# Kernel optimization log

Measured on AMD Instinct MI355X. Metric: run time of the kernel, lower is better.

## Reference

```python
import jax, jax.numpy as jnp
import numpy as np

N_NODES = 50000
N_EDGES = 800000
IN_CH, HID, OUT_CH, HEADS = 128, 32, 32, 8
NEG_SLOPE = 0.2


def setup_inputs() -> dict:
    key = jax.random.key(0)
    ks = jax.random.split(key, 20)
    x = jax.random.normal(ks[0], (N_NODES, IN_CH), dtype=jnp.float32)
    edge_index = jax.random.randint(ks[1], (2, N_EDGES), 0, N_NODES, dtype=jnp.int64)
    s = 0.1
    # encoder layer 1: in -> hid, heads=8 (concat)
    W1 = jax.random.normal(ks[2], (IN_CH, HEADS * HID), jnp.float32) * s
    as1 = jax.random.normal(ks[3], (HEADS, HID), jnp.float32) * s
    ad1 = jax.random.normal(ks[4], (HEADS, HID), jnp.float32) * s
    b1 = jnp.zeros((HEADS * HID,), jnp.float32)
    # encoder layer 2: hid*heads -> out, heads=1
    W2 = jax.random.normal(ks[5], (HEADS * HID, OUT_CH), jnp.float32) * s
    as2 = jax.random.normal(ks[6], (1, OUT_CH), jnp.float32) * s
    ad2 = jax.random.normal(ks[7], (1, OUT_CH), jnp.float32) * s
    b2 = jnp.zeros((OUT_CH,), jnp.float32)
    # decoder layer 1: out -> hid, heads=8 (concat)
    W3 = jax.random.normal(ks[8], (OUT_CH, HEADS * HID), jnp.float32) * s
    as3 = jax.random.normal(ks[9], (HEADS, HID), jnp.float32) * s
    ad3 = jax.random.normal(ks[10], (HEADS, HID), jnp.float32) * s
    b3 = jnp.zeros((HEADS * HID,), jnp.float32)
    # decoder layer 2: hid*heads -> in, heads=1
    W4 = jax.random.normal(ks[11], (HEADS * HID, IN_CH), jnp.float32) * s
    as4 = jax.random.normal(ks[12], (1, IN_CH), jnp.float32) * s
    ad4 = jax.random.normal(ks[13], (1, IN_CH), jnp.float32) * s
    b4 = jnp.zeros((IN_CH,), jnp.float32)
    return dict(x=x, edge_index=edge_index, W1=W1, as1=as1, ad1=ad1, b1=b1,
                W2=W2, as2=as2, ad2=ad2, b2=b2, W3=W3, as3=as3, ad3=ad3, b3=b3,
                W4=W4, as4=as4, ad4=ad4, b4=b4)


def gat_conv(x, src, dst, W, a_src, a_dst, b, heads, ch):
    # PyG GATConv: h = xW, e_ij = LeakyReLU(a_src.h_j + a_dst.h_i), softmax over incoming edges of i
    h = (x @ W).reshape(-1, heads, ch)                       # [N, H, C]
    al_s = jnp.sum(h * a_src[None], axis=-1)                 # [N, H]
    al_d = jnp.sum(h * a_dst[None], axis=-1)                 # [N, H]
    e = jax.nn.leaky_relu(al_s[src] + al_d[dst], NEG_SLOPE)  # [E, H]
    emax = jax.ops.segment_max(e, dst, num_segments=N_NODES)
    ee = jnp.exp(e - emax[dst])
    denom = jax.ops.segment_sum(ee, dst, num_segments=N_NODES)
    alpha = ee / denom[dst]                                  # [E, H]
    msg = alpha[:, :, None] * h[src]                         # [E, H, C]
    out = jax.ops.segment_sum(msg, dst, num_segments=N_NODES)  # [N, H, C]
    return out.reshape(N_NODES, heads * ch) + b


def reference(x, edge_index, W1, as1, ad1, b1, W2, as2, ad2, b2,
              W3, as3, ad3, b3, W4, as4, ad4, b4):
    # add self loops (PyG default add_self_loops=True)
    loop = jnp.arange(N_NODES, dtype=edge_index.dtype)
    src = jnp.concatenate([edge_index[0], loop])
    dst = jnp.concatenate([edge_index[1], loop])
    # encode
    z = gat_conv(x, src, dst, W1, as1, ad1, b1, HEADS, HID)
    z = jax.nn.relu(z)
    z = gat_conv(z, src, dst, W2, as2, ad2, b2, 1, OUT_CH)
    # decode
    r = gat_conv(z, src, dst, W3, as3, ad3, b3, HEADS, HID)
    r = jax.nn.relu(r)
    r = gat_conv(r, src, dst, W4, as4, ad4, b4, 1, IN_CH)
    return r
```

## Files before the change

kernel.cpp:

```cpp
#include <hip/hip_runtime.h>
#include <math.h>

#define N_NODES 50000
#define N_EDGES 800000
#define N_TOT   850000
#define NSB     ((N_NODES + 255) / 256)

typedef __attribute__((ext_vector_type(8))) short short8;
typedef __attribute__((ext_vector_type(4))) float floatx4;

__device__ __forceinline__ unsigned int pack_bf16x2(float a, float b) {
    unsigned ua = __float_as_uint(a);
    unsigned ub = __float_as_uint(b);
    ua += 0x7fff + ((ua >> 16) & 1);
    ub += 0x7fff + ((ub >> 16) & 1);
    return (ua >> 16) | (ub & 0xffff0000u);
}
__device__ __forceinline__ unsigned short pack_bf16(float a) {
    unsigned ua = __float_as_uint(a);
    ua += 0x7fff + ((ua >> 16) & 1);
    return (unsigned short)(ua >> 16);
}
__device__ __forceinline__ float bf16_lo(unsigned u) { return __uint_as_float(u << 16); }
__device__ __forceinline__ float bf16_hi(unsigned u) { return __uint_as_float(u & 0xffff0000u); }

__global__ void zero_int_kernel(int* p, int n) {
    int i = blockIdx.x * blockDim.x + threadIdx.x;
    if (i < n) p[i] = 0;
}

__global__ void deg_hist_kernel(const int* __restrict__ ei, int* __restrict__ deg) {
    int e = blockIdx.x * blockDim.x + threadIdx.x;
    if (e >= N_TOT) return;
    int dst = (e < N_EDGES) ? ei[N_EDGES + e] : (e - N_EDGES);
    atomicAdd(&deg[dst], 1);
}

__global__ void block_scan_kernel(const int* __restrict__ deg, int* __restrict__ part,
                                  int* __restrict__ bsum) {
    __shared__ int tmp[256];
    int t = threadIdx.x;
    int i = blockIdx.x * 256 + t;
    int v = (i < N_NODES) ? deg[i] : 0;
    tmp[t] = v;
    __syncthreads();
    for (int d = 1; d < 256; d <<= 1) {
        int u = (t >= d) ? tmp[t - d] : 0;
        __syncthreads();
        tmp[t] += u;
        __syncthreads();
    }
    if (i < N_NODES) part[i] = tmp[t] - v;
    if (t == 255) bsum[blockIdx.x] = tmp[255];
}

__global__ void scan_bsum_kernel(int* __restrict__ bsum) {
    __shared__ int tmp[256];
    int t = threadIdx.x;
    int v = (t < NSB) ? bsum[t] : 0;
    tmp[t] = v;
    __syncthreads();
    for (int d = 1; d < 256; d <<= 1) {
        int u = (t >= d) ? tmp[t - d] : 0;
        __syncthreads();
        tmp[t] += u;
        __syncthreads();
    }
    if (t < NSB) bsum[t] = tmp[t] - v;
}

__global__ void finalize_off_kernel(const int* __restrict__ part, const int* __restrict__ bsum,
                                    int* __restrict__ off, int* __restrict__ cursor) {
    int i = blockIdx.x * 256 + threadIdx.x;
    if (i < N_NODES) {
        int o = part[i] + bsum[blockIdx.x];
        off[i] = o;
        cursor[i] = o;
    }
    if (i == 0) off[N_NODES] = N_TOT;
}

__global__ void fill_csr_kernel(const int* __restrict__ ei, int* __restrict__ cursor,
                                int* __restrict__ csr_src) {
    int e = blockIdx.x * blockDim.x + threadIdx.x;
    if (e >= N_TOT) return;
    int src, dst;
    if (e < N_EDGES) { src = ei[e]; dst = ei[N_EDGES + e]; }
    else             { src = dst = e - N_EDGES; }
    int pos = atomicAdd(&cursor[dst], 1);
    csr_src[pos] = src;
}

__global__ void wconv_kernel(const float* __restrict__ W1, const float* __restrict__ W2,
                             const float* __restrict__ W3, const float* __restrict__ W4,
                             unsigned short* __restrict__ T1, unsigned short* __restrict__ T2,
                             unsigned short* __restrict__ T3, unsigned short* __restrict__ T4) {
    int i = blockIdx.x * 256 + threadIdx.x;
    const float* W; unsigned short* T; int K, N, idx;
    if      (i < 32768) { W = W1; T = T1; K = 128; N = 256; idx = i; }
    else if (i < 40960) { W = W2; T = T2; K = 256; N = 32;  idx = i - 32768; }
    else if (i < 49152) { W = W3; T = T3; K = 32;  N = 256; idx = i - 40960; }
    else if (i < 81920) { W = W4; T = T4; K = 256; N = 128; idx = i - 49152; }
    else return;
    int n = idx / K, k = idx % K;
    T[idx] = pack_bf16(W[(size_t)k * N + n]);
}

template<int Cin, int Cout, int H, int C, int NPB, int NW_N, bool IN_BF16>
__global__ void gemm_mfma_kernel(const void* __restrict__ xin,
                                 const unsigned short* __restrict__ Wt,
                                 const float* __restrict__ a_src, const float* __restrict__ a_dst,
                                 unsigned short* __restrict__ hb,
                                 float* __restrict__ al_s, float* __restrict__ al_d) {
    constexpr int NW_M = 4 / NW_N;
    constexpr int MT_W = (NPB / 16) / NW_M;
    constexpr int NT_W = (Cout / 16) / NW_N;
    constexpr int AS   = Cin + 8;
    constexpr int SP   = Cout + 4;
    __shared__ unsigned short xs[NPB * AS];
    __shared__ float hs[NPB * SP];
    int tid = threadIdx.x;
    int n0  = blockIdx.x * NPB;

    if (IN_BF16) {
        for (int i = tid; i < NPB * Cin / 8; i += 256) {
            int n = i / (Cin / 8), k8 = i % (Cin / 8);
            uint4 q = make_uint4(0u, 0u, 0u, 0u);
            if (n0 + n < N_NODES)
                q = ((const uint4*)((const unsigned short*)xin + (size_t)(n0 + n) * Cin))[k8];
            *(uint4*)(xs + n * AS + k8 * 8) = q;
        }
    } else {
        for (int i = tid; i < NPB * Cin / 4; i += 256) {
            int n = i / (Cin / 4), k4 = i % (Cin / 4);
            float4 v = make_float4(0.f, 0.f, 0.f, 0.f);
            if (n0 + n < N_NODES)
                v = ((const float4*)((const float*)xin + (size_t)(n0 + n) * Cin))[k4];
            uint2 p;
            p.x = pack_bf16x2(v.x, v.y);
            p.y = pack_bf16x2(v.z, v.w);
            *(uint2*)(xs + n * AS + k4 * 4) = p;
        }
    }
    __syncthreads();

    int w = tid >> 6, lane = tid & 63;
    int q = lane >> 4, l16 = lane & 15;
    int wm = w / NW_N, wn = w % NW_N;
    int mbase = wm * MT_W * 16;
    int nbase = wn * NT_W * 16;

    floatx4 acc[MT_W][NT_W];
#pragma unroll
    for (int mt = 0; mt < MT_W; mt++)
#pragma unroll
        for (int nt = 0; nt < NT_W; nt++) acc[mt][nt] = (floatx4){0.f, 0.f, 0.f, 0.f};

#pragma unroll
    for (int k0 = 0; k0 < Cin; k0 += 32) {
        short8 a[MT_W], b[NT_W];
#pragma unroll
        for (int mt = 0; mt < MT_W; mt++)
            a[mt] = *(const short8*)(xs + (mbase + mt * 16 + l16) * AS + k0 + q * 8);
#pragma unroll
        for (int nt = 0; nt < NT_W; nt++)
            b[nt] = *(const short8*)(Wt + (size_t)(nbase + nt * 16 + l16) * Cin + k0 + q * 8);
#pragma unroll
        for (int mt = 0; mt < MT_W; mt++)
#pragma unroll
            for (int nt = 0; nt < NT_W; nt++)
                acc[mt][nt] = __builtin_amdgcn_mfma_f32_16x16x32_bf16(a[mt], b[nt], acc[mt][nt], 0, 0, 0);
    }

#pragma unroll
    for (int mt = 0; mt < MT_W; mt++)
#pragma unroll
        for (int nt = 0; nt < NT_W; nt++)
#pragma unroll
            for (int r = 0; r < 4; r++) {
                int nl = mbase + mt * 16 + q * 4 + r;
                int ch = nbase + nt * 16 + l16;
                hs[nl * SP + ch] = acc[mt][nt][r];
            }
    __syncthreads();

    constexpr int TPN = Cout / 32;
    constexpr int TPH = (C > 32) ? (C / 32) : 1;
    if (tid < NPB * TPN) {
        int node = tid / TPN, sub = tid % TPN;
        int gn = n0 + node;
        int head = (sub * 32) / C;
        int coff = (sub * 32) % C;
        const float* hrow = hs + node * SP + sub * 32;
        const float* ap = a_src + head * C + coff;
        const float* dp = a_dst + head * C + coff;
        float ps = 0.f, pd = 0.f;
#pragma unroll
        for (int c4 = 0; c4 < 8; c4++) {
            float4 hv = *(const float4*)(hrow + c4 * 4);
            float4 av = *(const float4*)(ap + c4 * 4);
            float4 dv = *(const float4*)(dp + c4 * 4);
            ps += hv.x * av.x + hv.y * av.y + hv.z * av.z + hv.w * av.w;
            pd += hv.x * dv.x + hv.y * dv.y + hv.z * dv.z + hv.w * dv.w;
        }
        uint4 o0, o1;
        {
            float4 h0 = *(const float4*)(hrow + 0);
            float4 h1 = *(const float4*)(hrow + 4);
            float4 h2 = *(const float4*)(hrow + 8);
            float4 h3 = *(const float4*)(hrow + 12);
            o0.x = pack_bf16x2(h0.x, h0.y); o0.y = pack_bf16x2(h0.z, h0.w);
            o0.z = pack_bf16x2(h1.x, h1.y); o0.w = pack_bf16x2(h1.z, h1.w);
            o1.x = pack_bf16x2(h2.x, h2.y); o1.y = pack_bf16x2(h2.z, h2.w);
            o1.z = pack_bf16x2(h3.x, h3.y); o1.w = pack_bf16x2(h3.z, h3.w);
        }
        uint4 o2, o3;
        {
            float4 h0 = *(const float4*)(hrow + 16);
            float4 h1 = *(const float4*)(hrow + 20);
            float4 h2 = *(const float4*)(hrow + 24);
            float4 h3 = *(const float4*)(hrow + 28);
            o2.x = pack_bf16x2(h0.x, h0.y); o2.y = pack_bf16x2(h0.z, h0.w);
            o2.z = pack_bf16x2(h1.x, h1.y); o2.w = pack_bf16x2(h1.z, h1.w);
            o3.x = pack_bf16x2(h2.x, h2.y); o3.y = pack_bf16x2(h2.z, h2.w);
            o3.z = pack_bf16x2(h3.x, h3.y); o3.w = pack_bf16x2(h3.z, h3.w);
        }
        if (gn < N_NODES) {
            uint2* dst = (uint2*)(hb + (size_t)gn * Cout + sub * 32);
            dst[0] = make_uint2(o0.x, o0.y); dst[1] = make_uint2(o0.z, o0.w);
            dst[2] = make_uint2(o1.x, o1.y); dst[3] = make_uint2(o1.z, o1.w);
            dst[4] = make_uint2(o2.x, o2.y); dst[5] = make_uint2(o2.z, o2.w);
            dst[6] = make_uint2(o3.x, o3.y); dst[7] = make_uint2(o3.z, o3.w);
        }
        if (TPH > 1) {
#pragma unroll
            for (int k = 1; k < TPH; k <<= 1) {
                ps += __shfl_xor(ps, k, 64);
                pd += __shfl_xor(pd, k, 64);
            }
            if ((sub % TPH) == 0 && gn < N_NODES) {
                al_s[gn * H + head] = ps;
                al_d[gn * H + head] = pd;
            }
        } else {
            if (gn < N_NODES) {
                al_s[gn * H + head] = ps;
                al_d[gn * H + head] = pd;
            }
        }
    }
}

template<int H, int C, bool RELU, bool OUT_BF16>
__launch_bounds__(256, 6)
__global__ void gat_agg_kernel(const unsigned short* __restrict__ hb,
                               const float* __restrict__ al_s,
                               const float* __restrict__ al_d, const int* __restrict__ off,
                               const int* __restrict__ csr_src, const float* __restrict__ bias,
                               void* __restrict__ out) {
    constexpr int HC  = H * C;
    constexpr int G   = HC / 4;
    constexpr int SUB = G / H;
    constexpr int EB  = (SUB > 8) ? 8 : SUB;
    constexpr int NPW = 64 / G;
    constexpr int NPB = 4 * NPW;

    int tid  = threadIdx.x;
    int wid  = tid >> 6;
    int lane = tid & 63;
    int gi   = lane / G;
    int g    = lane % G;
    int node = blockIdx.x * NPB + wid * NPW + gi;
    if (node >= N_NODES) return;

    int head = g / SUB;
    int es   = g % EB;
    int nb   = lane & ~(G - 1);
    int r0 = off[node], r1 = off[node + 1];
    float ald = al_d[node * H + head];

    const uint2* hb2 = (const uint2*)hb;
    float4 acc = make_float4(0.f, 0.f, 0.f, 0.f);
    float wsum = 0.f;

    int j0 = r0;
    int idx0 = j0 + es;
    int sC = csr_src[(idx0 < r1) ? idx0 : (r1 - 1)];
    float eC = al_s[sC * H + head] + ald;

    for (; j0 + EB <= r1; j0 += EB) {
        int idxn = j0 + EB + es;
        int sN = csr_src[(idxn < r1) ? idxn : (r1 - 1)];
        float eL = fmaxf(eC, 0.2f * eC);
        float wC = __expf(eL);
        float eN = al_s[sN * H + head] + ald;
#pragma unroll
        for (int u = 0; u < EB; u++) {
            float wu = __shfl(wC, nb + head * EB + u, 64);
            int su = (NPW == 1) ? __builtin_amdgcn_readlane(sC, u)
                                : __shfl(sC, nb + u, 64);
            uint2 q = hb2[(size_t)su * G + g];
            wsum += wu;
            acc.x += wu * bf16_lo(q.x); acc.y += wu * bf16_hi(q.x);
            acc.z += wu * bf16_lo(q.y); acc.w += wu * bf16_hi(q.y);
        }
        sC = sN; eC = eN;
    }
    if (j0 < r1) {
        bool valid = (j0 + es) < r1;
        float eL = fmaxf(eC, 0.2f * eC);
        float wC = valid ? __expf(eL) : 0.f;
#pragma unroll
        for (int u = 0; u < EB; u++) {
            float wu = __shfl(wC, nb + head * EB + u, 64);
            if (wu != 0.f) {
                int su = (NPW == 1) ? __builtin_amdgcn_readlane(sC, u)
                                    : __shfl(sC, nb + u, 64);
                uint2 q = hb2[(size_t)su * G + g];
                wsum += wu;
                acc.x += wu * bf16_lo(q.x); acc.y += wu * bf16_hi(q.x);
                acc.z += wu * bf16_lo(q.y); acc.w += wu * bf16_hi(q.y);
            }
        }
    }

    float inv = 1.f / wsum;
    float4 bv = ((const float4*)bias)[g];
    acc.x = acc.x * inv + bv.x;
    acc.y = acc.y * inv + bv.y;
    acc.z = acc.z * inv + bv.z;
    acc.w = acc.w * inv + bv.w;
    if (RELU) {
        acc.x = fmaxf(acc.x, 0.f); acc.y = fmaxf(acc.y, 0.f);
        acc.z = fmaxf(acc.z, 0.f); acc.w = fmaxf(acc.w, 0.f);
    }
    if (OUT_BF16) {
        uint2 p;
        p.x = pack_bf16x2(acc.x, acc.y);
        p.y = pack_bf16x2(acc.z, acc.w);
        ((uint2*)out)[(size_t)node * (HC / 4) + g] = p;
    } else {
        ((float4*)out)[(size_t)node * (HC / 4) + g] = acc;
    }
}

extern "C" void kernel_launch(void* const* d_in, const int* in_sizes, int n_in,
                              void* d_out, int out_size, void* d_ws, size_t ws_size,
                              hipStream_t stream) {
    const float* x   = (const float*)d_in[0];
    const int*   ei  = (const int*)d_in[1];
    const float* W1  = (const float*)d_in[2];
    const float* as1 = (const float*)d_in[3];
    const float* ad1 = (const float*)d_in[4];
    const float* b1  = (const float*)d_in[5];
    const float* W2  = (const float*)d_in[6];
    const float* as2 = (const float*)d_in[7];
    const float* ad2 = (const float*)d_in[8];
    const float* b2  = (const float*)d_in[9];
    const float* W3  = (const float*)d_in[10];
    const float* as3 = (const float*)d_in[11];
    const float* ad3 = (const float*)d_in[12];
    const float* b3  = (const float*)d_in[13];
    const float* W4  = (const float*)d_in[14];
    const float* as4 = (const float*)d_in[15];
    const float* ad4 = (const float*)d_in[16];
    const float* b4  = (const float*)d_in[17];

    char* ws = (char*)d_ws;
    size_t o = 0;
    auto alloc = [&](size_t bytes) -> void* {
        void* p = ws + o;
        o = (o + bytes + 255) & ~(size_t)255;
        return p;
    };
    unsigned short* feat_a  = (unsigned short*)alloc((size_t)N_NODES * 256 * 2);
    unsigned short* feat_b  = (unsigned short*)alloc((size_t)N_NODES * 32 * 2);
    unsigned short* h_buf   = (unsigned short*)alloc((size_t)N_NODES * 256 * 2);
    float*          al_s    = (float*)alloc((size_t)N_NODES * 8 * 4);
    float*          al_d    = (float*)alloc((size_t)N_NODES * 8 * 4);
    int*            deg     = (int*)alloc((size_t)(N_NODES + 1) * 4);
    int*            off     = (int*)alloc((size_t)(N_NODES + 1) * 4);
    int*            cursor  = (int*)alloc((size_t)N_NODES * 4);
    int*            part    = (int*)alloc((size_t)N_NODES * 4);
    int*            bsum    = (int*)alloc((size_t)256 * 4);
    int*            csr_src = (int*)alloc((size_t)N_TOT * 4);
    unsigned short* w1t     = (unsigned short*)alloc(32768 * 2);
    unsigned short* w2t     = (unsigned short*)alloc(8192 * 2);
    unsigned short* w3t     = (unsigned short*)alloc(8192 * 2);
    unsigned short* w4t     = (unsigned short*)alloc(32768 * 2);

    const int TPB = 256;
    int nb_nodes = (N_NODES + TPB - 1) / TPB;
    int nb_edges = (N_TOT + TPB - 1) / TPB;

    zero_int_kernel<<<nb_nodes, TPB, 0, stream>>>(deg, N_NODES);
    wconv_kernel<<<320, TPB, 0, stream>>>(W1, W2, W3, W4, w1t, w2t, w3t, w4t);
    deg_hist_kernel<<<nb_edges, TPB, 0, stream>>>(ei, deg);
    block_scan_kernel<<<NSB, TPB, 0, stream>>>(deg, part, bsum);
    scan_bsum_kernel<<<1, TPB, 0, stream>>>(bsum);
    finalize_off_kernel<<<NSB, TPB, 0, stream>>>(part, bsum, off, cursor);
    fill_csr_kernel<<<nb_edges, TPB, 0, stream>>>(ei, cursor, csr_src);

    auto agg_blocks = [](int hc) { return (N_NODES * (hc / 4) + 255) / 256; };

    gemm_mfma_kernel<128, 256, 8, 32, 32, 4, false>
        <<<(N_NODES + 31) / 32, TPB, 0, stream>>>(x, w1t, as1, ad1, h_buf, al_s, al_d);
    gat_agg_kernel<8, 32, true, true><<<agg_blocks(256), TPB, 0, stream>>>(h_buf, al_s, al_d, off, csr_src, b1, feat_a);

    gemm_mfma_kernel<256, 32, 1, 32, 64, 2, true>
        <<<(N_NODES + 63) / 64, TPB, 0, stream>>>(feat_a, w2t, as2, ad2, h_buf, al_s, al_d);
    gat_agg_kernel<1, 32, false, true><<<agg_blocks(32), TPB, 0, stream>>>(h_buf, al_s, al_d, off, csr_src, b2, feat_b);

    gemm_mfma_kernel<32, 256, 8, 32, 32, 4, true>
        <<<(N_NODES + 31) / 32, TPB, 0, stream>>>(feat_b, w3t, as3, ad3, h_buf, al_s, al_d);
    gat_agg_kernel<8, 32, true, true><<<agg_blocks(256), TPB, 0, stream>>>(h_buf, al_s, al_d, off, csr_src, b3, feat_a);

    gemm_mfma_kernel<256, 128, 1, 128, 32, 4, true>
        <<<(N_NODES + 31) / 32, TPB, 0, stream>>>(feat_a, w4t, as4, ad4, h_buf, al_s, al_d);
    gat_agg_kernel<1, 128, false, false><<<agg_blocks(128), TPB, 0, stream>>>(h_buf, al_s, al_d, off, csr_src, b4, d_out);
}
```

Measured before the change: 483.6 us.

## Store projected features in slab-major layout and split aggregation by slab

The GEMM epilogue now writes projected bf16 features as 32-channel slabs (slab-major, node-minor) and attention logits head-major. The aggregation kernel launches one block group per slab, so each 8-lane group gathers only a 64-byte slab row per neighbour. Different blocks then work on different slabs, and the gather working set per slab is intended to fit better in cache. The cost is that edge indices and attention scores are re-read once per slab, and the launch-bounds occupancy hint is raised.

```diff
diff --git a/kernel.cpp b/kernel.cpp
--- a/kernel.cpp
+++ b/kernel.cpp
@@ -226,11 +226,8 @@
             o3.z = pack_bf16x2(h3.x, h3.y); o3.w = pack_bf16x2(h3.z, h3.w);
         }
         if (gn < N_NODES) {
-            uint2* dst = (uint2*)(hb + (size_t)gn * Cout + sub * 32);
-            dst[0] = make_uint2(o0.x, o0.y); dst[1] = make_uint2(o0.z, o0.w);
-            dst[2] = make_uint2(o1.x, o1.y); dst[3] = make_uint2(o1.z, o1.w);
-            dst[4] = make_uint2(o2.x, o2.y); dst[5] = make_uint2(o2.z, o2.w);
-            dst[6] = make_uint2(o3.x, o3.y); dst[7] = make_uint2(o3.z, o3.w);
+            uint4* dst4 = (uint4*)(hb + ((size_t)sub * N_NODES + gn) * 32);
+            dst4[0] = o0; dst4[1] = o1; dst4[2] = o2; dst4[3] = o3;
         }
         if (TPH > 1) {
 #pragma unroll
@@ -239,67 +236,65 @@
                 pd += __shfl_xor(pd, k, 64);
             }
             if ((sub % TPH) == 0 && gn < N_NODES) {
-                al_s[gn * H + head] = ps;
-                al_d[gn * H + head] = pd;
+                al_s[(size_t)head * N_NODES + gn] = ps;
+                al_d[(size_t)head * N_NODES + gn] = pd;
             }
         } else {
             if (gn < N_NODES) {
-                al_s[gn * H + head] = ps;
-                al_d[gn * H + head] = pd;
+                al_s[(size_t)head * N_NODES + gn] = ps;
+                al_d[(size_t)head * N_NODES + gn] = pd;
             }
         }
     }
 }
 
-template<int H, int C, bool RELU, bool OUT_BF16>
-__launch_bounds__(256, 6)
+template<int H, int C, int NP, bool RELU, bool OUT_BF16>
+__launch_bounds__(256, 8)
 __global__ void gat_agg_kernel(const unsigned short* __restrict__ hb,
                                const float* __restrict__ al_s,
-                               const float* __restrict__ al_d, const int* __restrict__ off,
-                               const int* __restrict__ csr_src, const float* __restrict__ bias,
+                               const float* __restrict__ al_d,
+                               const int* __restrict__ off,
+                               const int* __restrict__ csr_src,
+                               const float* __restrict__ bias,
                                void* __restrict__ out) {
-    constexpr int HC  = H * C;
-    constexpr int G   = HC / 4;
-    constexpr int SUB = G / H;
-    constexpr int EB  = (SUB > 8) ? 8 : SUB;
-    constexpr int NPW = 64 / G;
-    constexpr int NPB = 4 * NPW;
-
+    constexpr int HC = H * C;
+    const int p   = blockIdx.x % NP;
+    const int nch = blockIdx.x / NP;
     int tid  = threadIdx.x;
+    int lane = tid & 63;
     int wid  = tid >> 6;
-    int lane = tid & 63;
-    int gi   = lane / G;
-    int g    = lane % G;
-    int node = blockIdx.x * NPB + wid * NPW + gi;
+    int gi   = lane >> 3;
+    int g    = lane & 7;
+    int node = nch * 32 + wid * 8 + gi;
     if (node >= N_NODES) return;
 
-    int head = g / SUB;
-    int es   = g % EB;
-    int nb   = lane & ~(G - 1);
+    const int head = (H > 1) ? p : 0;
+    const float* __restrict__ als_p = al_s + (size_t)head * N_NODES;
+    const uint2* __restrict__ hbp   = (const uint2*)hb + (size_t)p * N_NODES * 8;
+    int nb = lane & 56;
+
     int r0 = off[node], r1 = off[node + 1];
-    float ald = al_d[node * H + head];
-
-    const uint2* hb2 = (const uint2*)hb;
+    float ald = al_d[(size_t)head * N_NODES + node];
+
     float4 acc = make_float4(0.f, 0.f, 0.f, 0.f);
     float wsum = 0.f;
 
     int j0 = r0;
-    int idx0 = j0 + es;
+    int idx0 = j0 + g;
     int sC = csr_src[(idx0 < r1) ? idx0 : (r1 - 1)];
-    float eC = al_s[sC * H + head] + ald;
-
-    for (; j0 + EB <= r1; j0 += EB) {
-        int idxn = j0 + EB + es;
+    float eC = als_p[sC] + ald;
+
+    for (; j0 + 8 <= r1; j0 += 8) {
+        int idxn = j0 + 8 + g;
         int sN = csr_src[(idxn < r1) ? idxn : (r1 - 1)];
         float eL = fmaxf(eC, 0.2f * eC);
         float wC = __expf(eL);
-        float eN = al_s[sN * H + head] + ald;
-#pragma unroll
-        for (int u = 0; u < EB; u++) {
-            float wu = __shfl(wC, nb + head * EB + u, 64);
-            int su = (NPW == 1) ? __builtin_amdgcn_readlane(sC, u)
-                                : __shfl(sC, nb + u, 64);
-            uint2 q = hb2[(size_t)su * G + g];
+        float eN = als_p[sN] + ald;
+#pragma unroll
+        for (int u = 0; u < 8; u++) {
+            float wu = __shfl(wC, nb + u, 64);
+            int   su = __shfl(sC, nb + u, 64);
+            uint2 q = hbp[(size_t)su * 8 + g];
             wsum += wu;
             acc.x += wu * bf16_lo(q.x); acc.y += wu * bf16_hi(q.x);
             acc.z += wu * bf16_lo(q.y); acc.w += wu * bf16_hi(q.y);
@@ -307,16 +302,15 @@
         sC = sN; eC = eN;
     }
     if (j0 < r1) {
-        bool valid = (j0 + es) < r1;
+        bool valid = (j0 + g) < r1;
         float eL = fmaxf(eC, 0.2f * eC);
         float wC = valid ? __expf(eL) : 0.f;
 #pragma unroll
-        for (int u = 0; u < EB; u++) {
-            float wu = __shfl(wC, nb + head * EB + u, 64);
+        for (int u = 0; u < 8; u++) {
+            float wu = __shfl(wC, nb + u, 64);
             if (wu != 0.f) {
-                int su = (NPW == 1) ? __builtin_amdgcn_readlane(sC, u)
-                                    : __shfl(sC, nb + u, 64);
-                uint2 q = hb2[(size_t)su * G + g];
+                int su = __shfl(sC, nb + u, 64);
+                uint2 q = hbp[(size_t)su * 8 + g];
                 wsum += wu;
                 acc.x += wu * bf16_lo(q.x); acc.y += wu * bf16_hi(q.x);
                 acc.z += wu * bf16_lo(q.y); acc.w += wu * bf16_hi(q.y);
@@ -325,7 +319,7 @@
     }
 
     float inv = 1.f / wsum;
-    float4 bv = ((const float4*)bias)[g];
+    float4 bv = ((const float4*)bias)[p * 8 + g];
     acc.x = acc.x * inv + bv.x;
     acc.y = acc.y * inv + bv.y;
     acc.z = acc.z * inv + bv.z;
@@ -334,13 +328,14 @@
         acc.x = fmaxf(acc.x, 0.f); acc.y = fmaxf(acc.y, 0.f);
         acc.z = fmaxf(acc.z, 0.f); acc.w = fmaxf(acc.w, 0.f);
     }
+    size_t oidx = (size_t)node * (HC / 4) + p * 8 + g;
     if (OUT_BF16) {
-        uint2 p;
-        p.x = pack_bf16x2(acc.x, acc.y);
-        p.y = pack_bf16x2(acc.z, acc.w);
-        ((uint2*)out)[(size_t)node * (HC / 4) + g] = p;
+        uint2 pk;
+        pk.x = pack_bf16x2(acc.x, acc.y);
+        pk.y = pack_bf16x2(acc.z, acc.w);
+        ((uint2*)out)[oidx] = pk;
     } else {
-        ((float4*)out)[(size_t)node * (HC / 4) + g] = acc;
+        ((float4*)out)[oidx] = acc;
     }
 }
 
@@ -401,21 +396,25 @@
     finalize_off_kernel<<<NSB, TPB, 0, stream>>>(part, bsum, off, cursor);
     fill_csr_kernel<<<nb_edges, TPB, 0, stream>>>(ei, cursor, csr_src);
 
-    auto agg_blocks = [](int hc) { return (N_NODES * (hc / 4) + 255) / 256; };
+    const int NBC = (N_NODES + 31) / 32;
 
     gemm_mfma_kernel<128, 256, 8, 32, 32, 4, false>
         <<<(N_NODES + 31) / 32, TPB, 0, stream>>>(x, w1t, as1, ad1, h_buf, al_s, al_d);
-    gat_agg_kernel<8, 32, true, true><<<agg_blocks(256), TPB, 0, stream>>>(h_buf, al_s, al_d, off, csr_src, b1, feat_a);
+    gat_agg_kernel<8, 32, 8, true, true>
+        <<<8 * NBC, TPB, 0, stream>>>(h_buf, al_s, al_d, off, csr_src, b1, feat_a);
 
     gemm_mfma_kernel<256, 32, 1, 32, 64, 2, true>
         <<<(N_NODES + 63) / 64, TPB, 0, stream>>>(feat_a, w2t, as2, ad2, h_buf, al_s, al_d);
-    gat_agg_kernel<1, 32, false, true><<<agg_blocks(32), TPB, 0, stream>>>(h_buf, al_s, al_d, off, csr_src, b2, feat_b);
+    gat_agg_kernel<1, 32, 1, false, true>
+        <<<NBC, TPB, 0, stream>>>(h_buf, al_s, al_d, off, csr_src, b2, feat_b);
 
     gemm_mfma_kernel<32, 256, 8, 32, 32, 4, true>
         <<<(N_NODES + 31) / 32, TPB, 0, stream>>>(feat_b, w3t, as3, ad3, h_buf, al_s, al_d);
-    gat_agg_kernel<8, 32, true, true><<<agg_blocks(256), TPB, 0, stream>>>(h_buf, al_s, al_d, off, csr_src, b3, feat_a);
+    gat_agg_kernel<8, 32, 8, true, true>
+        <<<8 * NBC, TPB, 0, stream>>>(h_buf, al_s, al_d, off, csr_src, b3, feat_a);
 
     gemm_mfma_kernel<256, 128, 1, 128, 32, 4, true>
         <<<(N_NODES + 31) / 32, TPB, 0, stream>>>(feat_a, w4t, as4, ad4, h_buf, al_s, al_d);
-    gat_agg_kernel<1, 128, false, false><<<agg_blocks(128), TPB, 0, stream>>>(h_buf, al_s, al_d, off, csr_src, b4, d_out);
-}
+    gat_agg_kernel<1, 128, 4, false, false>
+        <<<4 * NBC, TPB, 0, stream>>>(h_buf, al_s, al_d, off, csr_src, b4, d_out);
+}
```

Result: slower. 519.0 us (+7.3%).

## Sort nodes by degree within 256-node windows to balance multi-node aggregation waves

Applied to the files above, without the earlier changes.

Adds a kernel that counting-sorts each 256-node window by in-degree into a permutation. Aggregation kernels that pack several nodes per wavefront then process nodes in that order, so lanes in a wave have similar edge counts and wait less on the longest-degree node. It costs one extra small kernel launch plus an indirect perm lookup, and output writes become slightly scattered within each window.

```diff
diff --git a/kernel.cpp b/kernel.cpp
--- a/kernel.cpp
+++ b/kernel.cpp
@@ -104,6 +104,36 @@
     else return;
     int n = idx / K, k = idx % K;
     T[idx] = pack_bf16(W[(size_t)k * N + n]);
+}
+
+__global__ void window_sort_kernel(const int* __restrict__ deg, int* __restrict__ perm) {
+    __shared__ int lh[256];
+    __shared__ int sc[256];
+    __shared__ int lr[256];
+    int t = threadIdx.x;
+    int base = blockIdx.x * 256;
+    int i = base + t;
+    lh[t] = 0;
+    __syncthreads();
+    int d = 0;
+    bool valid = i < N_NODES;
+    if (valid) {
+        d = deg[i]; if (d > 255) d = 255;
+        lr[t] = atomicAdd(&lh[d], 1);
+    }
+    __syncthreads();
+    int v = lh[t];
+    sc[t] = v;
+    __syncthreads();
+    for (int s = 1; s < 256; s <<= 1) {
+        int u = (t >= s) ? sc[t - s] : 0;
+        __syncthreads();
+        sc[t] += u;
+        __syncthreads();
+    }
+    lh[t] = sc[t] - v;
+    __syncthreads();
+    if (valid) perm[base + lh[d] + lr[t]] = i;
 }
 
 template<int Cin, int Cout, int H, int C, int NPB, int NW_N, bool IN_BF16>
@@ -256,7 +286,9 @@
 __global__ void gat_agg_kernel(const unsigned short* __restrict__ hb,
                                const float* __restrict__ al_s,
                                const float* __restrict__ al_d, const int* __restrict__ off,
-                               const int* __restrict__ csr_src, const float* __restrict__ bias,
+                               const int* __restrict__ csr_src,
+                               const int* __restrict__ perm,
+                               const float* __restrict__ bias,
                                void* __restrict__ out) {
     constexpr int HC  = H * C;
     constexpr int G   = HC / 4;
@@ -270,8 +302,9 @@
     int lane = tid & 63;
     int gi   = lane / G;
     int g    = lane % G;
-    int node = blockIdx.x * NPB + wid * NPW + gi;
-    if (node >= N_NODES) return;
+    int ni   = blockIdx.x * NPB + wid * NPW + gi;
+    if (ni >= N_NODES) return;
+    int node = (NPW > 1) ? perm[ni] : ni;
 
     int head = g / SUB;
     int es   = g % EB;
@@ -299,7 +332,7 @@
             float wu = __shfl(wC, nb + head * EB + u, 64);
             int su = (NPW == 1) ? __builtin_amdgcn_readlane(sC, u)
                                 : __shfl(sC, nb + u, 64);
-            uint2 q = hb2[(size_t)su * G + g];
+            uint2 q = hb2[(size_t)su * (HC / 4) + g];
             wsum += wu;
             acc.x += wu * bf16_lo(q.x); acc.y += wu * bf16_hi(q.x);
             acc.z += wu * bf16_lo(q.y); acc.w += wu * bf16_hi(q.y);
@@ -316,7 +349,7 @@
             if (wu != 0.f) {
                 int su = (NPW == 1) ? __builtin_amdgcn_readlane(sC, u)
                                     : __shfl(sC, nb + u, 64);
-                uint2 q = hb2[(size_t)su * G + g];
+                uint2 q = hb2[(size_t)su * (HC / 4) + g];
                 wsum += wu;
                 acc.x += wu * bf16_lo(q.x); acc.y += wu * bf16_hi(q.x);
                 acc.z += wu * bf16_lo(q.y); acc.w += wu * bf16_hi(q.y);
@@ -384,6 +417,7 @@
     int*            part    = (int*)alloc((size_t)N_NODES * 4);
     int*            bsum    = (int*)alloc((size_t)256 * 4);
     int*            csr_src = (int*)alloc((size_t)N_TOT * 4);
+    int*            perm    = (int*)alloc((size_t)N_NODES * 4);
     unsigned short* w1t     = (unsigned short*)alloc(32768 * 2);
     unsigned short* w2t     = (unsigned short*)alloc(8192 * 2);
     unsigned short* w3t     = (unsigned short*)alloc(8192 * 2);
@@ -396,6 +430,7 @@
     zero_int_kernel<<<nb_nodes, TPB, 0, stream>>>(deg, N_NODES);
     wconv_kernel<<<320, TPB, 0, stream>>>(W1, W2, W3, W4, w1t, w2t, w3t, w4t);
     deg_hist_kernel<<<nb_edges, TPB, 0, stream>>>(ei, deg);
+    window_sort_kernel<<<NSB, TPB, 0, stream>>>(deg, perm);
     block_scan_kernel<<<NSB, TPB, 0, stream>>>(deg, part, bsum);
     scan_bsum_kernel<<<1, TPB, 0, stream>>>(bsum);
     finalize_off_kernel<<<NSB, TPB, 0, stream>>>(part, bsum, off, cursor);
@@ -405,17 +440,17 @@
 
     gemm_mfma_kernel<128, 256, 8, 32, 32, 4, false>
         <<<(N_NODES + 31) / 32, TPB, 0, stream>>>(x, w1t, as1, ad1, h_buf, al_s, al_d);
-    gat_agg_kernel<8, 32, true, true><<<agg_blocks(256), TPB, 0, stream>>>(h_buf, al_s, al_d, off, csr_src, b1, feat_a);
+    gat_agg_kernel<8, 32, true, true><<<agg_blocks(256), TPB, 0, stream>>>(h_buf, al_s, al_d, off, csr_src, perm, b1, feat_a);
 
     gemm_mfma_kernel<256, 32, 1, 32, 64, 2, true>
         <<<(N_NODES + 63) / 64, TPB, 0, stream>>>(feat_a, w2t, as2, ad2, h_buf, al_s, al_d);
-    gat_agg_kernel<1, 32, false, true><<<agg_blocks(32), TPB, 0, stream>>>(h_buf, al_s, al_d, off, csr_src, b2, feat_b);
+    gat_agg_kernel<1, 32, false, true><<<agg_blocks(32), TPB, 0, stream>>>(h_buf, al_s, al_d, off, csr_src, perm, b2, feat_b);
 
     gemm_mfma_kernel<32, 256, 8, 32, 32, 4, true>
         <<<(N_NODES + 31) / 32, TPB, 0, stream>>>(feat_b, w3t, as3, ad3, h_buf, al_s, al_d);
-    gat_agg_kernel<8, 32, true, true><<<agg_blocks(256), TPB, 0, stream>>>(h_buf, al_s, al_d, off, csr_src, b3, feat_a);
+    gat_agg_kernel<8, 32, true, true><<<agg_blocks(256), TPB, 0, stream>>>(h_buf, al_s, al_d, off, csr_src, perm, b3, feat_a);
 
     gemm_mfma_kernel<256, 128, 1, 128, 32, 4, true>
         <<<(N_NODES + 31) / 32, TPB, 0, stream>>>(feat_a, w4t, as4, ad4, h_buf, al_s, al_d);
-    gat_agg_kernel<1, 128, false, false><<<agg_blocks(128), TPB, 0, stream>>>(h_buf, al_s, al_d, off, csr_src, b4, d_out);
-}
+    gat_agg_kernel<1, 128, false, false><<<agg_blocks(128), TPB, 0, stream>>>(h_buf, al_s, al_d, off, csr_src, perm, b4, d_out);
+}
```

Result: no change. 486.5 us (+0.6%).
